# Performance work log

Hardware: AMD Instinct MI355X
Metric: run time of the kernel (lower is better)

Reference implementation:

```python
import jax, jax.numpy as jnp
from jax import lax
import numpy as np

TAU = 10.0      # tauSr == tauRef
THR = 1.0       # theta
WIDTH = 1.0     # tauRho (surrogate width)
SCALE = 1.0     # scaleRho (surrogate scale)
DECAY = float(np.exp(-1.0 / TAU))


@jax.custom_vjp
def _heaviside(v):
    # spike = 1[v >= theta]
    return (v >= THR).astype(v.dtype)

def _heaviside_fwd(v):
    return _heaviside(v), v

def _heaviside_bwd(v, g):
    # SLAYER exponential surrogate pdf: scaleRho/tauRho * exp(-|v-theta|/tauRho)
    return (g * (SCALE / WIDTH) * jnp.exp(-jnp.abs(v - THR) / WIDTH),)

_heaviside.defvjp(_heaviside_fwd, _heaviside_bwd)


def _conv2d(x, w, pad):
    # x: (B, Cin, H, W), w: (Cout, Cin, kh, kw); SLAYER convs have no bias
    return lax.conv_general_dilated(
        x, w, window_strides=(1, 1), padding=[(pad, pad), (pad, pad)],
        dimension_numbers=("NCHW", "OIHW", "NCHW"))


def _sumpool(x, k):
    # SLAYER pool = sum over kxk window (times a learned scalar applied outside)
    B, C, H, W = x.shape
    return x.reshape(B, C, H // k, k, W // k, k).sum(axis=(3, 5))


def _psp(seq):
    # exponential synaptic (PSP) filter along time: s[t] = a*s[t-1] + x[t]
    a = jnp.asarray(DECAY, seq.dtype)
    def step(s, x_t):
        s = a * s + x_t
        return s, s
    _, out = lax.scan(step, jnp.zeros_like(seq[0]), seq)
    return out  # (T, ...)


def _spikes(u):
    # thresholded spiking with decaying refractory feedback (scaleRef=1):
    # v[t] = u[t] - r[t]; s[t] = 1[v >= theta]; r[t+1] = b*(r[t] + theta*s[t])
    b = jnp.asarray(DECAY, u.dtype)
    def step(r, u_t):
        s = _heaviside(u_t - r)
        r_next = b * (r + THR * s)
        return r_next, s
    _, out = lax.scan(step, jnp.zeros_like(u[0]), u)
    return out  # (T, ...)


def _forward(x, conv1_w, conv2_w, lin_w, w_pool1, w_pool2):
    N, T, C, H, W = x.shape  # (64, 100, 2, 32, 32)
    h = _conv2d(x.reshape(N * T, C, H, W), conv1_w, 2)        # (NT, 4, 32, 32)
    h = _sumpool(h, 4) * w_pool1                               # (NT, 4, 8, 8)
    h = h.reshape(N, T, 4, 8, 8).swapaxes(0, 1)                # (T, N, 4, 8, 8)
    s1 = _spikes(_psp(h))                                      # (T, N, 4, 8, 8)
    h2 = _conv2d(s1.reshape(T * N, 4, 8, 8), conv2_w, 1)       # (TN, 8, 8, 8)
    h2 = (_sumpool(h2, 2) * w_pool2).reshape(T, N, 8, 4, 4)    # (T, N, 8, 4, 4)
    s2 = _spikes(_psp(h2))                                     # (T, N, 8, 4, 4)
    # dense = full-spatial conv (2, 8, 4, 4) -> (N, T, 2)
    return jnp.einsum("tnchw,ochw->nto", s2, lin_w)


def setup_inputs() -> dict:
    key = jax.random.key(0)
    ks = jax.random.split(key, 4)
    x = (jax.random.uniform(ks[0], (64, 100, 2, 32, 32)) < 0.1).astype(jnp.float32)
    conv1_w = jax.random.normal(ks[1], (4, 2, 5, 5), jnp.float32) * 0.3
    conv2_w = jax.random.normal(ks[2], (8, 4, 3, 3), jnp.float32) * 0.3
    lin_w = jax.random.normal(ks[3], (2, 8, 4, 4), jnp.float32) * 0.3
    w_pool1 = jnp.float32(1.0 / 16.0)  # 1.1*theta / (16 * 1.1)
    w_pool2 = jnp.float32(1.0 / 4.0)   # 1.1*theta / (4 * 1.1)
    return {"x": x, "conv1_w": conv1_w, "conv2_w": conv2_w, "lin_w": lin_w,
            "w_pool1": w_pool1, "w_pool2": w_pool2}


def reference(x, conv1_w, conv2_w, lin_w, w_pool1, w_pool2):
    return _forward(x, conv1_w, conv2_w, lin_w, w_pool1, w_pool2)
```

## Files before the change

kernel.cpp:

```cpp
#include <hip/hip_runtime.h>


#define DECAY 0.9048374180359595f

#define BAR_LGKM() asm volatile("s_waitcnt lgkmcnt(0)\n\ts_barrier" ::: "memory")
#define FENCE_LGKM() asm volatile("s_waitcnt lgkmcnt(0)" ::: "memory")

__global__ __launch_bounds__(128) void k0_fold(const float* __restrict__ w1,
        const float* __restrict__ w2, const float* __restrict__ wp1,
        const float* __restrict__ wp2, float* __restrict__ wl1,
        float* __restrict__ wl2, float* __restrict__ out) {
    const int tid = threadIdx.x;
    out[blockIdx.x * 128 + tid] = 0.f;
    if (blockIdx.x != 0) return;
    const float p1 = wp1[0], p2 = wp2[0];
    for (int idx = tid; idx < 512; idx += 128) {
        const int f = idx & 7, c = (idx >> 3) & 3, e = (idx >> 5) & 7, cin = idx >> 8;
        const int cc = c * 2 + cin;
        int alo = e - 3; if (alo < 0) alo = 0;
        int ahi = e;     if (ahi > 4) ahi = 4;
        int blo = f - 3; if (blo < 0) blo = 0;
        int bhi = f;     if (bhi > 4) bhi = 4;
        float s = 0.f;
        for (int a = alo; a <= ahi; ++a)
            for (int b = blo; b <= bhi; ++b)
                s += w1[cc * 25 + a * 5 + b];
        wl1[(cin * 8 + e) * 32 + c * 8 + f] = s * p1;
    }
    for (int idx = tid; idx < 512; idx += 128) {
        const int c2 = idx & 7, f = (idx >> 3) & 3, e = (idx >> 5) & 3, cin = idx >> 7;
        int alo = e - 1; if (alo < 0) alo = 0;
        int ahi = e;     if (ahi > 2) ahi = 2;
        int blo = f - 1; if (blo < 0) blo = 0;
        int bhi = f;     if (bhi > 2) bhi = 2;
        float s = 0.f;
        for (int aa = alo; aa <= ahi; ++aa)
            for (int bb = blo; bb <= bhi; ++bb)
                s += w2[((c2 * 4 + cin) * 3 + aa) * 3 + bb];
        wl2[c2 * 68 + cin * 16 + e * 4 + f] = s * p2;
    }
}

__global__ __launch_bounds__(64) void k1(const float* __restrict__ x,
        const float* __restrict__ wg, float* __restrict__ u1) {
    __shared__ __align__(16) float xs[2 * 1296];
    __shared__ __align__(16) float wl[512];
    const int lane = threadIdx.x;
    const int frame = blockIdx.x;
    const int n = frame / 100, t = frame % 100;

    *(float4*)(wl + 4 * lane)       = *(const float4*)(wg + 4 * lane);
    *(float4*)(wl + 256 + 4 * lane) = *(const float4*)(wg + 256 + 4 * lane);

    #pragma unroll
    for (int m0 = 0; m0 < 128; m0 += 64) {
        const int m = m0 + lane;
        if (m < 72) {
            const int cin = m / 36, rem = m % 36;
            const int rr = rem / 9, q4 = rem % 9;
            const int pr = (rr == 0) ? 0 : (rr == 1) ? 9 : (rr == 2) ? 26 : 35;
            *(float4*)(xs + cin * 1296 + pr * 36 + q4 * 4) = make_float4(0.f, 0.f, 0.f, 0.f);
        }
    }
    #pragma unroll
    for (int m0 = 0; m0 < 192; m0 += 64) {
        const int m = m0 + lane;
        if (m < 144) {
            const int cin = m / 72, rem = m % 72;
            const int side = rem & 1, pr = rem >> 1;
            *(float2*)(xs + cin * 1296 + pr * 36 + side * 34) = make_float2(0.f, 0.f);
        }
    }
    const float4* xg = (const float4*)(x + (size_t)frame * 2048);
    #pragma unroll
    for (int q = 0; q < 8; ++q) {
        const int m = q * 64 + lane;
        const float4 v = xg[m];
        const int li = 4 * m;
        const int cin = li >> 10, row = (li >> 5) & 31, col = li & 31;
        const int r = row + 2;
        const int pr = (r & 3) * 9 + (r >> 2);
        float* d = xs + cin * 1296 + pr * 36 + col + 2;
        *(float2*)(d)     = make_float2(v.x, v.y);
        *(float2*)(d + 2) = make_float2(v.z, v.w);
    }
    FENCE_LGKM();

    const int cp = lane >> 5;
    const int i  = (lane >> 2) & 7;
    const int jh = (lane >> 1) & 1;
    const int eh = lane & 1;

    float acc[2][4] = {{0.f, 0.f, 0.f, 0.f}, {0.f, 0.f, 0.f, 0.f}};
    const float* tb = xs + (i + eh) * 36 + jh * 16;
    #pragma unroll
    for (int cin = 0; cin < 2; ++cin) {
        #pragma unroll
        for (int et = 0; et < 4; ++et) {
            const int ro = cin * 1296 + et * 9 * 36;
            float xr[20];
            #pragma unroll
            for (int b = 0; b < 5; ++b)
                *(float4*)(xr + 4 * b) = *(const float4*)(tb + ro + 4 * b);
            float wv[16];
            const float* wp = wl + (cin * 8 + eh * 4 + et) * 32 + cp * 16;
            #pragma unroll
            for (int q = 0; q < 4; ++q)
                *(float4*)(wv + 4 * q) = *(const float4*)(wp + 4 * q);
            #pragma unroll
            for (int cl = 0; cl < 2; ++cl) {
                #pragma unroll
                for (int jj = 0; jj < 4; ++jj) {
                    const int o = 4 * jj;
                    acc[cl][jj] += xr[o]*wv[cl*8]     + xr[o+1]*wv[cl*8+1]
                                 + xr[o+2]*wv[cl*8+2] + xr[o+3]*wv[cl*8+3]
                                 + xr[o+4]*wv[cl*8+4] + xr[o+5]*wv[cl*8+5]
                                 + xr[o+6]*wv[cl*8+6] + xr[o+7]*wv[cl*8+7];
                }
            }
        }
    }
    #pragma unroll
    for (int cl = 0; cl < 2; ++cl)
        #pragma unroll
        for (int jj = 0; jj < 4; ++jj)
            acc[cl][jj] += __shfl_xor(acc[cl][jj], 1);

    const float o0 = eh ? acc[1][0] : acc[0][0];
    const float o1 = eh ? acc[1][1] : acc[0][1];
    const float o2 = eh ? acc[1][2] : acc[0][2];
    const float o3 = eh ? acc[1][3] : acc[0][3];
    *(float4*)(u1 + (size_t)t * 16384 + n * 256 + (2 * cp + eh) * 64 + i * 8 + jh * 4) =
        make_float4(o0, o1, o2, o3);
}

__global__ __launch_bounds__(256) void kf(const float* __restrict__ u1,
        const float* __restrict__ wl2g, const float* __restrict__ lw,
        float* __restrict__ out) {
    __shared__ __align__(16) float ls1[8 * 660];
    __shared__ __align__(16) float ls2[8 * 68];
    const int tid = threadIdx.x;
    const int n = blockIdx.x >> 1, h = blockIdx.x & 1;
    const int wave = tid >> 6, l64 = tid & 63;
    const float a = DECAY;

    for (int m = tid; m < 1320; m += 256)
        *(float4*)(ls1 + 4 * m) = make_float4(0.f, 0.f, 0.f, 0.f);

    const int cs = tid >> 6, rowi = (tid >> 3) & 7, col = tid & 7;
    const int pr1 = (((rowi + 1) & 1) * 5) + ((rowi + 1) >> 1);
    const int woff = cs * 160 + pr1 * 16 + 1 + col;
    const float* up = u1 + n * 256 + tid;

    const int sub = tid >> 4, l16 = tid & 15;
    const int c2l = l16 >> 2, i2 = l16 & 3;
    const int c2g = h * 4 + c2l;

    float4 wreg[16];
    {
        const float* wbase = wl2g + c2g * 68;
        #pragma unroll
        for (int q = 0; q < 16; ++q)
            wreg[q] = *(const float4*)(wbase + (q >> 2) * 16 + (q & 3) * 4);
    }

    const float dw0 = lw[h * 64 + l64];
    const float dw1 = lw[128 + h * 64 + l64];

    float psp = 0.f, rr = 0.f;
    float psp2 = 0.f, rr2 = 0.f;

    float vbuf[8];
    #pragma unroll
    for (int k = 0; k < 8; ++k) vbuf[k] = up[(size_t)k * 16384];

    BAR_LGKM();

    #pragma unroll 1
    for (int rd = 0; rd < 13; ++rd) {
        const int t0 = rd * 8;
        const int cnt = (rd == 12) ? 4 : 8;

        float sreg[8];
        #pragma unroll
        for (int k = 0; k < 8; ++k) {
            if (k < cnt) {
                psp = a * psp + vbuf[k];
                const float vv = psp - rr;
                const float s = (vv >= 1.f) ? 1.f : 0.f;
                rr = a * (rr + s);
                sreg[k] = s;
            }
        }
        #pragma unroll
        for (int k = 0; k < 8; ++k) {
            const int tt = t0 + 8 + k;
            if (tt < 100) vbuf[k] = up[(size_t)tt * 16384];
        }
        #pragma unroll
        for (int k = 0; k < 8; ++k)
            if (k < cnt) ls1[k * 660 + woff] = sreg[k];
        BAR_LGKM();

        if (tid < 128 && sub < cnt) {
            const float* tb = ls1 + sub * 660 + i2 * 16;
            float acc[4] = {0.f, 0.f, 0.f, 0.f};
            #pragma unroll
            for (int cin = 0; cin < 4; ++cin) {
                #pragma unroll
                for (int e = 0; e < 4; ++e) {
                    const int C = cin * 160 + ((e & 1) * 5 + (e >> 1)) * 16;
                    float xr[12];
                    #pragma unroll
                    for (int b = 0; b < 3; ++b)
                        *(float4*)(xr + 4 * b) = *(const float4*)(tb + C + 4 * b);
                    const float4 wf = wreg[cin * 4 + e];
                    #pragma unroll
                    for (int j = 0; j < 4; ++j) {
                        acc[j] += xr[2 * j]     * wf.x;
                        acc[j] += xr[2 * j + 1] * wf.y;
                        acc[j] += xr[2 * j + 2] * wf.z;
                        acc[j] += xr[2 * j + 3] * wf.w;
                    }
                }
            }
            *(float4*)(ls2 + sub * 68 + c2l * 16 + i2 * 4) =
                make_float4(acc[0], acc[1], acc[2], acc[3]);
        }
        BAR_LGKM();

        if (tid < 64) {
            #pragma unroll
            for (int k = 0; k < 8; ++k) {
                if (k < cnt) {
                    const float u = ls2[k * 68 + tid];
                    psp2 = a * psp2 + u;
                    const float vv = psp2 - rr2;
                    const float s = (vv >= 1.f) ? 1.f : 0.f;
                    rr2 = a * (rr2 + s);
                    ls2[k * 68 + tid] = s;
                }
            }
        }
        BAR_LGKM();

        #pragma unroll
        for (int hh = 0; hh < 2; ++hh) {
            const int ss = wave + 4 * hh;
            if (ss < cnt) {
                const float sa = ls2[ss * 68 + l64];
                float a0 = sa * dw0;
                float a1 = sa * dw1;
                #pragma unroll
                for (int off = 32; off > 0; off >>= 1) {
                    a0 += __shfl_down(a0, off);
                    a1 += __shfl_down(a1, off);
                }
                if (l64 == 0) {
                    const int tt = t0 + ss;
                    atomicAdd(&out[n * 200 + tt * 2],     a0);
                    atomicAdd(&out[n * 200 + tt * 2 + 1], a1);
                }
            }
        }
    }
}

extern "C" void kernel_launch(void* const* d_in, const int* in_sizes, int n_in,
                              void* d_out, int out_size, void* d_ws, size_t ws_size,
                              hipStream_t stream) {
    const float* x   = (const float*)d_in[0];
    const float* w1  = (const float*)d_in[1];
    const float* w2  = (const float*)d_in[2];
    const float* lw  = (const float*)d_in[3];
    const float* wp1 = (const float*)d_in[4];
    const float* wp2 = (const float*)d_in[5];

    float* u1  = (float*)d_ws;
    float* wl1 = u1 + 1638400;
    float* wl2 = wl1 + 512;
    float* out = (float*)d_out;

    k0_fold<<<100, 128, 0, stream>>>(w1, w2, wp1, wp2, wl1, wl2, out);
    k1<<<6400, 64, 0, stream>>>(x, wl1, u1);
    kf<<<128, 256, 0, stream>>>(u1, wl2, lw, out);
}
```

Baseline: 140.7 us.

## Split final kernel across four channel-quarters and process 16 timesteps per round

The final spiking kernel now launches four blocks per sample instead of two. Each block owns two output channels, and each round covers 16 timesteps instead of 8, which halves the number of barrier-separated rounds. The conv2 work is spread over all 256 threads with two outputs each. The second spike stage and the dense reduction are merged into a single wave, which removes one block barrier per round. In exchange, the layer-1 PSP/spike recurrence is recomputed redundantly in four blocks rather than two, and the kernel uses more LDS and more registers.

```diff
diff --git a/kernel.cpp b/kernel.cpp
--- a/kernel.cpp
+++ b/kernel.cpp
@@ -137,14 +137,14 @@
 __global__ __launch_bounds__(256) void kf(const float* __restrict__ u1,
         const float* __restrict__ wl2g, const float* __restrict__ lw,
         float* __restrict__ out) {
-    __shared__ __align__(16) float ls1[8 * 660];
-    __shared__ __align__(16) float ls2[8 * 68];
+    __shared__ __align__(16) float ls1[16 * 660];
+    __shared__ __align__(16) float ls2[16 * 36];
     const int tid = threadIdx.x;
-    const int n = blockIdx.x >> 1, h = blockIdx.x & 1;
+    const int n = blockIdx.x >> 2, qtr = blockIdx.x & 3;
     const int wave = tid >> 6, l64 = tid & 63;
     const float a = DECAY;
 
-    for (int m = tid; m < 1320; m += 256)
+    for (int m = tid; m < 2640; m += 256)
         *(float4*)(ls1 + 4 * m) = make_float4(0.f, 0.f, 0.f, 0.f);
 
     const int cs = tid >> 6, rowi = (tid >> 3) & 7, col = tid & 7;
@@ -153,8 +153,8 @@
     const float* up = u1 + n * 256 + tid;
 
     const int sub = tid >> 4, l16 = tid & 15;
-    const int c2l = l16 >> 2, i2 = l16 & 3;
-    const int c2g = h * 4 + c2l;
+    const int c2l = l16 >> 3, i2 = (l16 >> 1) & 3, jhp = l16 & 1;
+    const int c2g = qtr * 2 + c2l;
 
     float4 wreg[16];
     {
@@ -164,26 +164,33 @@
             wreg[q] = *(const float4*)(wbase + (q >> 2) * 16 + (q & 3) * 4);
     }
 
-    const float dw0 = lw[h * 64 + l64];
-    const float dw1 = lw[128 + h * 64 + l64];
+    float dwA[8], dwB[8];
+    {
+        const int idx = l64 & 3;
+        #pragma unroll
+        for (int m = 0; m < 8; ++m) {
+            dwA[m] = lw[qtr * 32 + idx * 8 + m];
+            dwB[m] = lw[128 + qtr * 32 + idx * 8 + m];
+        }
+    }
 
     float psp = 0.f, rr = 0.f;
     float psp2 = 0.f, rr2 = 0.f;
 
-    float vbuf[8];
-    #pragma unroll
-    for (int k = 0; k < 8; ++k) vbuf[k] = up[(size_t)k * 16384];
+    float vbuf[16];
+    #pragma unroll
+    for (int k = 0; k < 16; ++k) vbuf[k] = up[(size_t)k * 16384];
 
     BAR_LGKM();
 
     #pragma unroll 1
-    for (int rd = 0; rd < 13; ++rd) {
-        const int t0 = rd * 8;
-        const int cnt = (rd == 12) ? 4 : 8;
-
-        float sreg[8];
-        #pragma unroll
-        for (int k = 0; k < 8; ++k) {
+    for (int rd = 0; rd < 7; ++rd) {
+        const int t0 = rd * 16;
+        const int cnt = (rd == 6) ? 4 : 16;
+
+        float sreg[16];
+        #pragma unroll
+        for (int k = 0; k < 16; ++k) {
             if (k < cnt) {
                 psp = a * psp + vbuf[k];
                 const float vv = psp - rr;
@@ -193,71 +200,66 @@
             }
         }
         #pragma unroll
-        for (int k = 0; k < 8; ++k) {
-            const int tt = t0 + 8 + k;
+        for (int k = 0; k < 16; ++k) {
+            const int tt = t0 + 16 + k;
             if (tt < 100) vbuf[k] = up[(size_t)tt * 16384];
         }
         #pragma unroll
-        for (int k = 0; k < 8; ++k)
+        for (int k = 0; k < 16; ++k)
             if (k < cnt) ls1[k * 660 + woff] = sreg[k];
         BAR_LGKM();
 
-        if (tid < 128 && sub < cnt) {
-            const float* tb = ls1 + sub * 660 + i2 * 16;
-            float acc[4] = {0.f, 0.f, 0.f, 0.f};
+        if (sub < cnt) {
+            const float* tb = ls1 + sub * 660 + i2 * 16 + 4 * jhp;
+            float acc0 = 0.f, acc1 = 0.f;
             #pragma unroll
             for (int cin = 0; cin < 4; ++cin) {
                 #pragma unroll
                 for (int e = 0; e < 4; ++e) {
                     const int C = cin * 160 + ((e & 1) * 5 + (e >> 1)) * 16;
-                    float xr[12];
-                    #pragma unroll
-                    for (int b = 0; b < 3; ++b)
-                        *(float4*)(xr + 4 * b) = *(const float4*)(tb + C + 4 * b);
+                    float xr[6];
+                    *(float4*)(xr)     = *(const float4*)(tb + C);
+                    *(float2*)(xr + 4) = *(const float2*)(tb + C + 4);
                     const float4 wf = wreg[cin * 4 + e];
-                    #pragma unroll
-                    for (int j = 0; j < 4; ++j) {
-                        acc[j] += xr[2 * j]     * wf.x;
-                        acc[j] += xr[2 * j + 1] * wf.y;
-                        acc[j] += xr[2 * j + 2] * wf.z;
-                        acc[j] += xr[2 * j + 3] * wf.w;
+                    acc0 += xr[0] * wf.x; acc0 += xr[1] * wf.y;
+                    acc0 += xr[2] * wf.z; acc0 += xr[3] * wf.w;
+                    acc1 += xr[2] * wf.x; acc1 += xr[3] * wf.y;
+                    acc1 += xr[4] * wf.z; acc1 += xr[5] * wf.w;
+                }
+            }
+            *(float2*)(ls2 + sub * 36 + c2l * 16 + i2 * 4 + 2 * jhp) =
+                make_float2(acc0, acc1);
+        }
+        BAR_LGKM();
+
+        if (wave == 0) {
+            if (l64 < 32) {
+                #pragma unroll
+                for (int k = 0; k < 16; ++k) {
+                    if (k < cnt) {
+                        const float u = ls2[k * 36 + l64];
+                        psp2 = a * psp2 + u;
+                        const float vv = psp2 - rr2;
+                        const float s = (vv >= 1.f) ? 1.f : 0.f;
+                        rr2 = a * (rr2 + s);
+                        ls2[k * 36 + l64] = s;
                     }
                 }
             }
-            *(float4*)(ls2 + sub * 68 + c2l * 16 + i2 * 4) =
-                make_float4(acc[0], acc[1], acc[2], acc[3]);
-        }
-        BAR_LGKM();
-
-        if (tid < 64) {
-            #pragma unroll
-            for (int k = 0; k < 8; ++k) {
-                if (k < cnt) {
-                    const float u = ls2[k * 68 + tid];
-                    psp2 = a * psp2 + u;
-                    const float vv = psp2 - rr2;
-                    const float s = (vv >= 1.f) ? 1.f : 0.f;
-                    rr2 = a * (rr2 + s);
-                    ls2[k * 68 + tid] = s;
-                }
-            }
-        }
-        BAR_LGKM();
-
-        #pragma unroll
-        for (int hh = 0; hh < 2; ++hh) {
-            const int ss = wave + 4 * hh;
-            if (ss < cnt) {
-                const float sa = ls2[ss * 68 + l64];
-                float a0 = sa * dw0;
-                float a1 = sa * dw1;
-                #pragma unroll
-                for (int off = 32; off > 0; off >>= 1) {
-                    a0 += __shfl_down(a0, off);
-                    a1 += __shfl_down(a1, off);
-                }
-                if (l64 == 0) {
-                    const int tt = t0 + ss;
+            FENCE_LGKM();
+            const int slot = l64 >> 2, idx = l64 & 3;
+            if (slot < cnt) {
+                float a0 = 0.f, a1 = 0.f;
+                #pragma unroll
+                for (int m = 0; m < 8; ++m) {
+                    const float s = ls2[slot * 36 + idx * 8 + m];
+                    a0 += s * dwA[m];
+                    a1 += s * dwB[m];
+                }
+                a0 += __shfl_down(a0, 2); a0 += __shfl_down(a0, 1);
+                a1 += __shfl_down(a1, 2); a1 += __shfl_down(a1, 1);
+                if (idx == 0) {
+                    const int tt = t0 + slot;
                     atomicAdd(&out[n * 200 + tt * 2],     a0);
                     atomicAdd(&out[n * 200 + tt * 2 + 1], a1);
                 }
@@ -283,5 +285,5 @@
 
     k0_fold<<<100, 128, 0, stream>>>(w1, w2, wp1, wp2, wl1, wl2, out);
     k1<<<6400, 64, 0, stream>>>(x, wl1, u1);
-    kf<<<128, 256, 0, stream>>>(u1, wl2, lw, out);
-}
+    kf<<<256, 256, 0, stream>>>(u1, wl2, lw, out);
+}
```

Result: faster. 123.9 us (-12.0%).
